# Kernel optimization log

Hardware: AMD Instinct MI355X
Metric: run time of the kernel (lower is better)

Reference implementation:

```python
import jax, jax.numpy as jnp
import numpy as np

U = 512  # units

def hard_sigmoid(x):
    # Keras hard_sigmoid: clip(0.2*x + 0.5, 0, 1)
    return jnp.clip(0.2 * x + 0.5, 0.0, 1.0)

def setup_inputs() -> dict:
    key = jax.random.key(0)
    ks = jax.random.split(key, 9)
    B, T, A, D = 64, 2048, 512, 512  # batch, annotation steps, annotation units, input dim
    s = lambda k, shape, scale: jax.random.normal(k, shape, jnp.float32) * scale
    return {
        "inputs": s(ks[0], (B, D), 1.0),
        "h": s(ks[1], (B, U), 1.0),
        "c": s(ks[2], (B, U), 1.0),
        "annotations": s(ks[3], (B, T, A), 1.0),
        "kernel": s(ks[4], (D + A, 4 * U), 0.02),
        "recurrent_kernel": s(ks[5], (U, 4 * U), 0.02),
        "bias": jnp.zeros((6 * U,), jnp.float32).at[U:2 * U].set(1.0),  # unit_forget_bias
        "kernel_u": s(ks[6], (A, U), 0.02),
        "kernel_w": s(ks[7], (U, U), 0.02),
        "kernel_v": s(ks[8], (U,), 0.02),
    }

def reference(inputs, h, c, annotations, kernel, recurrent_kernel, bias, kernel_u, kernel_w, kernel_v):
    bias_u = bias[4 * U:5 * U]
    # precomputed annotation projection (done once in build()): [B,T,U]
    uh = jnp.einsum('bta,au->btu', annotations, kernel_u) + bias_u
    # Bahdanau attention scores
    Wxstm = h @ kernel_w                                   # [B,U]
    et = jnp.einsum('btu,u->bt', jnp.tanh(uh + Wxstm[:, None, :]), kernel_v)
    at = jax.nn.softmax(et, axis=1)                        # exp/sum in source == softmax
    context = jnp.einsum('bt,bta->ba', at, annotations)    # [B,A]
    x = jnp.concatenate([inputs, context], axis=-1)        # [B, D+A]
    z = x @ kernel + h @ recurrent_kernel + bias[:4 * U]   # [B,4U]
    i = hard_sigmoid(z[:, :U])
    f = hard_sigmoid(z[:, U:2 * U])
    c_new = f * c + i * jnp.tanh(z[:, 2 * U:3 * U])
    o = hard_sigmoid(z[:, 3 * U:])
    h_new = o * jnp.tanh(c_new)
    return h_new
```

## Files before the change

### kernel.cpp

```cpp
#include <hip/hip_runtime.h>

constexpr int U = 512;
constexpr int B = 64;
constexpr int T = 2048;
constexpr int A = 512;

typedef __attribute__((ext_vector_type(8))) short short8;
typedef __attribute__((ext_vector_type(4))) float f32x4;

__device__ __forceinline__ unsigned short f32_to_bf16(float f) {
    unsigned int b = __float_as_uint(f);
    unsigned int r = (b + 0x7FFFu + ((b >> 16) & 1u)) >> 16;
    return (unsigned short)r;
}

__device__ __forceinline__ float fast_tanh(float x) {
    float e = exp2f(x * 2.885390081777927f);
    return (e - 1.0f) * __builtin_amdgcn_rcpf(e + 1.0f);
}

__device__ __forceinline__ float hard_sigmoid(float z) {
    return fminf(fmaxf(0.2f * z + 0.5f, 0.0f), 1.0f);
}

__global__ __launch_bounds__(256) void k_prep_s(const float* __restrict__ h,
                                                const float* __restrict__ kw,
                                                float* __restrict__ Sp) {
    int b = blockIdx.x >> 2;
    int kc = blockIdx.x & 3;
    int u = threadIdx.x;
    const float* hb = h + b * U + kc * 128;
    const float* kwb = kw + (size_t)kc * 128 * U;
    float a0 = 0.f, a1 = 0.f;
#pragma unroll 4
    for (int k = 0; k < 128; ++k) {
        float hv = hb[k];
        a0 += hv * kwb[(size_t)k * U + u];
        a1 += hv * kwb[(size_t)k * U + u + 256];
    }
    float* p = Sp + ((size_t)kc * 64 + b) * U;
    p[u] = a0;
    p[u + 256] = a1;
}

__global__ __launch_bounds__(256) void k_s_reduce(const float* __restrict__ Sp,
                                                  const float* __restrict__ bias,
                                                  float* __restrict__ S) {
    int gid = blockIdx.x * 256 + threadIdx.x;
    int b = gid >> 9, u = gid & 511;
    float s = bias[4 * U + u];
#pragma unroll
    for (int kc = 0; kc < 4; ++kc) s += Sp[((size_t)kc * 64 + b) * U + u];
    S[gid] = s;
}

__global__ __launch_bounds__(256) void k_prep_kut(const float* __restrict__ ku,
                                                  unsigned short* __restrict__ kut) {
    __shared__ float tile[32][33];
    int a0 = (blockIdx.x >> 4) << 5;
    int u0 = (blockIdx.x & 15) << 5;
    int c = threadIdx.x & 31, r0 = threadIdx.x >> 5;
#pragma unroll
    for (int p = 0; p < 4; ++p) {
        int r = r0 + p * 8;
        tile[r][c] = ku[(a0 + r) * U + u0 + c];
    }
    __syncthreads();
#pragma unroll
    for (int p = 0; p < 4; ++p) {
        int r = r0 + p * 8;
        kut[(u0 + r) * A + a0 + c] = f32_to_bf16(tile[c][r]);
    }
}

__global__ __launch_bounds__(256) void k_prep_wt(const float* __restrict__ kern,
                                                 const float* __restrict__ rk,
                                                 unsigned short* __restrict__ Wt) {
    __shared__ float tile[32][33];
    int k0 = blockIdx.x << 5;
    int j0 = blockIdx.y << 5;
    int c = threadIdx.x & 31, r0 = threadIdx.x >> 5;
#pragma unroll
    for (int p = 0; p < 4; ++p) {
        int r = r0 + p * 8;
        int k = k0 + r;
        float val = (k < 1024) ? kern[k * 2048 + j0 + c]
                               : rk[(k - 1024) * 2048 + j0 + c];
        tile[r][c] = val;
    }
    __syncthreads();
#pragma unroll
    for (int p = 0; p < 4; ++p) {
        int r = r0 + p * 8;
        Wt[(size_t)(j0 + r) * 1536 + k0 + c] = f32_to_bf16(tile[c][r]);
    }
}

__global__ __launch_bounds__(256, 2) void k_gemm_et(const float* __restrict__ ann,
                                                    const unsigned short* __restrict__ kut,
                                                    const float* __restrict__ S,
                                                    const float* __restrict__ v,
                                                    float* __restrict__ etp) {
    __shared__ unsigned short As[128 * 64];
    __shared__ unsigned short Bs[256 * 64];
    __shared__ float red[4][64];

    const int tid = threadIdx.x;
    const int wave = tid >> 6;
    const int lane = tid & 63;
    const int lanelo = lane & 15;
    const int quad = lane >> 4;
    const int wm = wave >> 1, wn = wave & 1;

    const int bid = blockIdx.x;
    const int nt = (bid >> 3) & 1;
    const int mt = (bid & 7) | ((bid >> 4) << 3);
    const int b = mt >> 4;
    const float* aBase = ann + (size_t)mt * 128 * A;
    const unsigned short* bBase = kut + (size_t)nt * 256 * A;

    f32x4 acc[4][8];
#pragma unroll
    for (int i = 0; i < 4; ++i)
#pragma unroll
        for (int j = 0; j < 8; ++j) acc[i][j] = {0.f, 0.f, 0.f, 0.f};

    for (int k0 = 0; k0 < A; k0 += 64) {
#pragma unroll
        for (int p = 0; p < 8; ++p) {
            int seg = p * 4 + wave;
            int flat = seg * 1024 + lane * 16;
            int row = flat >> 7;
            int sc = (flat >> 4) & 7;
            int d = sc ^ (row & 7);
            __builtin_amdgcn_global_load_lds(
                (const __attribute__((address_space(1))) void*)(bBase + (size_t)row * A + k0 + d * 8),
                (__attribute__((address_space(3))) void*)((char*)Bs + seg * 1024),
                16, 0, 0);
        }
#pragma unroll
        for (int p = 0; p < 4; ++p) {
            int flat8 = p * 256 + tid;
            int row = flat8 >> 3;
            int c8 = flat8 & 7;
            const float* src = aBase + (size_t)row * A + k0 + c8 * 8;
            f32x4 v0 = *(const f32x4*)src;
            f32x4 v1 = *(const f32x4*)(src + 4);
            short8 pk;
            pk[0] = (short)f32_to_bf16(v0.x);
            pk[1] = (short)f32_to_bf16(v0.y);
            pk[2] = (short)f32_to_bf16(v0.z);
            pk[3] = (short)f32_to_bf16(v0.w);
            pk[4] = (short)f32_to_bf16(v1.x);
            pk[5] = (short)f32_to_bf16(v1.y);
            pk[6] = (short)f32_to_bf16(v1.z);
            pk[7] = (short)f32_to_bf16(v1.w);
            *(short8*)&As[row * 64 + ((c8 ^ (row & 7)) * 8)] = pk;
        }
        __syncthreads();
#pragma unroll
        for (int s = 0; s < 2; ++s) {
            int c = s * 4 + quad;
            short8 af[4];
#pragma unroll
            for (int mi = 0; mi < 4; ++mi) {
                int row = wm * 64 + mi * 16 + lanelo;
                af[mi] = *(const short8*)&As[row * 64 + ((c ^ (row & 7)) * 8)];
            }
            short8 bfr[8];
#pragma unroll
            for (int ni = 0; ni < 8; ++ni) {
                int rowb = wn * 128 + ni * 16 + lanelo;
                bfr[ni] = *(const short8*)&Bs[rowb * 64 + ((c ^ (rowb & 7)) * 8)];
            }
#pragma unroll
            for (int mi = 0; mi < 4; ++mi)
#pragma unroll
                for (int ni = 0; ni < 8; ++ni)
                    acc[mi][ni] = __builtin_amdgcn_mfma_f32_16x16x32_bf16(
                        af[mi], bfr[ni], acc[mi][ni], 0, 0, 0);
        }
        __syncthreads();
    }

    float rows[16];
#pragma unroll
    for (int i = 0; i < 16; ++i) rows[i] = 0.f;
#pragma unroll
    for (int ni = 0; ni < 8; ++ni) {
        int n = nt * 256 + wn * 128 + ni * 16 + lanelo;
        float sv = S[b * U + n];
        float vv = v[n];
#pragma unroll
        for (int mi = 0; mi < 4; ++mi)
#pragma unroll
            for (int r = 0; r < 4; ++r)
                rows[mi * 4 + r] += fast_tanh(acc[mi][ni][r] + sv) * vv;
    }
#pragma unroll
    for (int i = 0; i < 16; ++i) {
        rows[i] += __shfl_xor(rows[i], 1);
        rows[i] += __shfl_xor(rows[i], 2);
        rows[i] += __shfl_xor(rows[i], 4);
        rows[i] += __shfl_xor(rows[i], 8);
    }
    if (lanelo == 0) {
#pragma unroll
        for (int mi = 0; mi < 4; ++mi)
#pragma unroll
            for (int r = 0; r < 4; ++r)
                red[wave][mi * 16 + quad * 4 + r] = rows[mi * 4 + r];
    }
    __syncthreads();
    if (tid < 128) {
        int wmv = tid >> 6, ml = tid & 63;
        float sum = red[wmv * 2][ml] + red[wmv * 2 + 1][ml];
        etp[(size_t)nt * (1024 * 128) + (size_t)mt * 128 + tid] = sum;
    }
}

__global__ __launch_bounds__(256) void k_softmax(const float* __restrict__ etp,
                                                 float* __restrict__ at) {
    __shared__ float sred[256];
    int b = blockIdx.x;
    const float* e = etp + b * T;
    float vals[8];
    float mx = -1e30f;
#pragma unroll
    for (int i = 0; i < 8; ++i) {
        int t = threadIdx.x + i * 256;
        float x = e[t] + e[131072 + t];
        vals[i] = x;
        mx = fmaxf(mx, x);
    }
    sred[threadIdx.x] = mx;
    __syncthreads();
    for (int s = 128; s > 0; s >>= 1) {
        if (threadIdx.x < s) sred[threadIdx.x] = fmaxf(sred[threadIdx.x], sred[threadIdx.x + s]);
        __syncthreads();
    }
    mx = sred[0];
    __syncthreads();
    float sum = 0.f;
#pragma unroll
    for (int i = 0; i < 8; ++i) {
        float x = exp2f((vals[i] - mx) * 1.4426950408889634f);
        vals[i] = x;
        sum += x;
    }
    sred[threadIdx.x] = sum;
    __syncthreads();
    for (int s = 128; s > 0; s >>= 1) {
        if (threadIdx.x < s) sred[threadIdx.x] += sred[threadIdx.x + s];
        __syncthreads();
    }
    float inv = 1.0f / sred[0];
#pragma unroll
    for (int i = 0; i < 8; ++i) at[b * T + threadIdx.x + i * 256] = vals[i] * inv;
}

__global__ __launch_bounds__(256) void k_ctx_part(const float* __restrict__ at,
                                                  const float* __restrict__ ann,
                                                  float* __restrict__ part) {
    __shared__ float buf[2][512];
    int b = blockIdx.x >> 3;
    int tc = blockIdx.x & 7;
    int half = threadIdx.x >> 7;
    int a4 = (threadIdx.x & 127) << 2;
    const float* annb = ann + ((size_t)b * T + tc * 256) * A;
    const float* atb = at + b * T + tc * 256;
    f32x4 acc = {0.f, 0.f, 0.f, 0.f};
    for (int t = half; t < 256; t += 2) {
        float w = atb[t];
        f32x4 rv = *(const f32x4*)(annb + (size_t)t * A + a4);
        acc.x += w * rv.x;
        acc.y += w * rv.y;
        acc.z += w * rv.z;
        acc.w += w * rv.w;
    }
    *(f32x4*)&buf[half][a4] = acc;
    __syncthreads();
    int a2 = threadIdx.x << 1;
    float s0 = buf[0][a2] + buf[1][a2];
    float s1 = buf[0][a2 + 1] + buf[1][a2 + 1];
    float* p = part + ((size_t)b * 8 + tc) * A;
    p[a2] = s0;
    p[a2 + 1] = s1;
}

__global__ __launch_bounds__(256) void k_ctx_reduce(const float* __restrict__ part,
                                                    float* __restrict__ ctx) {
    int b = blockIdx.x;
    for (int a = threadIdx.x; a < A; a += 256) {
        float s = 0.f;
#pragma unroll
        for (int c = 0; c < 8; ++c) s += part[((size_t)b * 8 + c) * A + a];
        ctx[b * A + a] = s;
    }
}

__global__ __launch_bounds__(256) void k_prep_xb(const float* __restrict__ inputs,
                                                 const float* __restrict__ ctx,
                                                 const float* __restrict__ h,
                                                 unsigned short* __restrict__ xb) {
    int b = blockIdx.y;
    int k = blockIdx.x * 256 + threadIdx.x;
    float val;
    if (k < 512) val = inputs[b * 512 + k];
    else if (k < 1024) val = ctx[b * 512 + (k - 512)];
    else val = h[b * 512 + (k - 1024)];
    xb[b * 1536 + k] = f32_to_bf16(val);
}

__global__ __launch_bounds__(256) void k_zgemm(const unsigned short* __restrict__ xb,
                                               const unsigned short* __restrict__ Wt,
                                               float* __restrict__ zpart) {
    const int kc = blockIdx.x & 7;
    const int nt = blockIdx.x >> 3;
    const int wave = threadIdx.x >> 6;
    const int lane = threadIdx.x & 63;
    const int lanelo = lane & 15;
    const int quad = lane >> 4;

    const int n = nt * 64 + wave * 16 + lanelo;
    const unsigned short* bp = Wt + (size_t)n * 1536 + kc * 192 + quad * 8;
    const unsigned short* ap = xb + (size_t)lanelo * 1536 + kc * 192 + quad * 8;

    f32x4 acc[4];
#pragma unroll
    for (int i = 0; i < 4; ++i) acc[i] = {0.f, 0.f, 0.f, 0.f};

#pragma unroll
    for (int ks = 0; ks < 6; ++ks) {
        short8 bfrag = *(const short8*)(bp + ks * 32);
#pragma unroll
        for (int mi = 0; mi < 4; ++mi) {
            short8 afrag = *(const short8*)(ap + (size_t)mi * 16 * 1536 + ks * 32);
            acc[mi] = __builtin_amdgcn_mfma_f32_16x16x32_bf16(afrag, bfrag, acc[mi], 0, 0, 0);
        }
    }

    float* p = zpart + (size_t)kc * 64 * 2048;
#pragma unroll
    for (int mi = 0; mi < 4; ++mi)
#pragma unroll
        for (int r = 0; r < 4; ++r) {
            int m = mi * 16 + quad * 4 + r;
            p[(size_t)m * 2048 + n] = acc[mi][r];
        }
}

__global__ __launch_bounds__(256) void k_gates(const float* __restrict__ zpart,
                                               const float* __restrict__ bias,
                                               const float* __restrict__ c,
                                               float* __restrict__ hnew) {
    int gid = blockIdx.x * 256 + threadIdx.x;
    int b = gid >> 9;
    int u = gid & 511;
    float z[4];
#pragma unroll
    for (int g = 0; g < 4; ++g) {
        int j = (g << 9) + u;
        float s = bias[j];
#pragma unroll
        for (int kc = 0; kc < 8; ++kc)
            s += zpart[((size_t)kc * 64 + b) * 2048 + j];
        z[g] = s;
    }
    float ig = hard_sigmoid(z[0]);
    float fg = hard_sigmoid(z[1]);
    float cn = fg * c[b * 512 + u] + ig * fast_tanh(z[2]);
    float og = hard_sigmoid(z[3]);
    hnew[b * 512 + u] = og * fast_tanh(cn);
}

extern "C" void kernel_launch(void* const* d_in, const int* in_sizes, int n_in,
                              void* d_out, int out_size, void* d_ws, size_t ws_size,
                              hipStream_t stream) {
    const float* inputs = (const float*)d_in[0];
    const float* h      = (const float*)d_in[1];
    const float* c      = (const float*)d_in[2];
    const float* ann    = (const float*)d_in[3];
    const float* kern   = (const float*)d_in[4];
    const float* rk     = (const float*)d_in[5];
    const float* bias   = (const float*)d_in[6];
    const float* ku     = (const float*)d_in[7];
    const float* kw     = (const float*)d_in[8];
    const float* kv     = (const float*)d_in[9];

    char* ws = (char*)d_ws;
    float*          S     = (float*)(ws + 0);
    unsigned short* kut   = (unsigned short*)(ws + 131072);
    float*          etp   = (float*)(ws + 655360);
    float*          at    = (float*)(ws + 1703936);
    float*          part  = (float*)(ws + 2228224);
    float*          Sp    = (float*)(ws + 2228224);
    float*          ctx   = (float*)(ws + 3276800);
    unsigned short* xb    = (unsigned short*)(ws + 3407872);
    unsigned short* Wt    = (unsigned short*)(ws + 3604480);
    float*          zpart = (float*)(ws + 9895936);
    float*          hnew  = (float*)d_out;

    k_prep_wt<<<dim3(48, 64), 256, 0, stream>>>(kern, rk, Wt);
    k_prep_kut<<<256, 256, 0, stream>>>(ku, kut);
    k_prep_s<<<256, 256, 0, stream>>>(h, kw, Sp);
    k_s_reduce<<<128, 256, 0, stream>>>(Sp, bias, S);
    k_gemm_et<<<2048, 256, 0, stream>>>(ann, kut, S, kv, etp);
    k_softmax<<<64, 256, 0, stream>>>(etp, at);
    k_ctx_part<<<64 * 8, 256, 0, stream>>>(at, ann, part);
    k_ctx_reduce<<<64, 256, 0, stream>>>(part, ctx);
    k_prep_xb<<<dim3(6, 64), 256, 0, stream>>>(inputs, ctx, h, xb);
    k_zgemm<<<256, 256, 0, stream>>>(xb, Wt, zpart);
    k_gates<<<128, 256, 0, stream>>>(zpart, bias, c, hnew);
}
```

Baseline: 516.7 us.

## Retile attention-score GEMM to full-N 64-row tiles with register prefetch

The et GEMM now gives each block 64 annotation rows against all 512 units instead of 128 rows against half the units. Each annotation row is therefore read and converted to bf16 only once, and the two-way partial score sum is gone, so softmax reads a single et buffer. The next k-slice of annotations is also prefetched into registers so the global load overlaps the MFMA loop. The cost is that the full kernel_u tile (64 KB of LDS) is now reloaded per block, and more LDS per block may reduce occupancy.

```diff
diff --git a/kernel.cpp b/kernel.cpp
--- a/kernel.cpp
+++ b/kernel.cpp
@@ -100,9 +100,9 @@
                                                     const unsigned short* __restrict__ kut,
                                                     const float* __restrict__ S,
                                                     const float* __restrict__ v,
-                                                    float* __restrict__ etp) {
-    __shared__ unsigned short As[128 * 64];
-    __shared__ unsigned short Bs[256 * 64];
+                                                    float* __restrict__ et) {
+    __shared__ unsigned short As[64 * 64];
+    __shared__ unsigned short Bs[512 * 64];
     __shared__ float red[4][64];
 
     const int tid = threadIdx.x;
@@ -110,14 +110,12 @@
     const int lane = tid & 63;
     const int lanelo = lane & 15;
     const int quad = lane >> 4;
-    const int wm = wave >> 1, wn = wave & 1;
-
-    const int bid = blockIdx.x;
-    const int nt = (bid >> 3) & 1;
-    const int mt = (bid & 7) | ((bid >> 4) << 3);
-    const int b = mt >> 4;
-    const float* aBase = ann + (size_t)mt * 128 * A;
-    const unsigned short* bBase = kut + (size_t)nt * 256 * A;
+    const int wn = wave;
+
+    const int mt = blockIdx.x;
+    const int b = mt >> 5;
+    const int t0 = (mt & 31) << 6;
+    const float* aBase = ann + (size_t)mt * 64 * A;
 
     f32x4 acc[4][8];
 #pragma unroll
@@ -125,27 +123,34 @@
 #pragma unroll
         for (int j = 0; j < 8; ++j) acc[i][j] = {0.f, 0.f, 0.f, 0.f};
 
+    f32x4 pv[4];
+    const int rowA = tid >> 3;
+    const int c8A = tid & 7;
+
+#pragma unroll
+    for (int q = 0; q < 2; ++q) {
+        const float* src = aBase + (size_t)(q * 32 + rowA) * A + 0 + c8A * 8;
+        pv[q * 2] = *(const f32x4*)src;
+        pv[q * 2 + 1] = *(const f32x4*)(src + 4);
+    }
+
     for (int k0 = 0; k0 < A; k0 += 64) {
 #pragma unroll
-        for (int p = 0; p < 8; ++p) {
+        for (int p = 0; p < 16; ++p) {
             int seg = p * 4 + wave;
             int flat = seg * 1024 + lane * 16;
             int row = flat >> 7;
             int sc = (flat >> 4) & 7;
             int d = sc ^ (row & 7);
             __builtin_amdgcn_global_load_lds(
-                (const __attribute__((address_space(1))) void*)(bBase + (size_t)row * A + k0 + d * 8),
+                (const __attribute__((address_space(1))) void*)(kut + (size_t)row * A + k0 + d * 8),
                 (__attribute__((address_space(3))) void*)((char*)Bs + seg * 1024),
                 16, 0, 0);
         }
 #pragma unroll
-        for (int p = 0; p < 4; ++p) {
-            int flat8 = p * 256 + tid;
-            int row = flat8 >> 3;
-            int c8 = flat8 & 7;
-            const float* src = aBase + (size_t)row * A + k0 + c8 * 8;
-            f32x4 v0 = *(const f32x4*)src;
-            f32x4 v1 = *(const f32x4*)(src + 4);
+        for (int q = 0; q < 2; ++q) {
+            int row = q * 32 + rowA;
+            f32x4 v0 = pv[q * 2], v1 = pv[q * 2 + 1];
             short8 pk;
             pk[0] = (short)f32_to_bf16(v0.x);
             pk[1] = (short)f32_to_bf16(v0.y);
@@ -155,16 +160,24 @@
             pk[5] = (short)f32_to_bf16(v1.y);
             pk[6] = (short)f32_to_bf16(v1.z);
             pk[7] = (short)f32_to_bf16(v1.w);
-            *(short8*)&As[row * 64 + ((c8 ^ (row & 7)) * 8)] = pk;
+            *(short8*)&As[row * 64 + ((c8A ^ (row & 7)) * 8)] = pk;
         }
         __syncthreads();
+        if (k0 + 64 < A) {
+#pragma unroll
+            for (int q = 0; q < 2; ++q) {
+                const float* src = aBase + (size_t)(q * 32 + rowA) * A + (k0 + 64) + c8A * 8;
+                pv[q * 2] = *(const f32x4*)src;
+                pv[q * 2 + 1] = *(const f32x4*)(src + 4);
+            }
+        }
 #pragma unroll
         for (int s = 0; s < 2; ++s) {
             int c = s * 4 + quad;
             short8 af[4];
 #pragma unroll
             for (int mi = 0; mi < 4; ++mi) {
-                int row = wm * 64 + mi * 16 + lanelo;
+                int row = mi * 16 + lanelo;
                 af[mi] = *(const short8*)&As[row * 64 + ((c ^ (row & 7)) * 8)];
             }
             short8 bfr[8];
@@ -188,9 +201,9 @@
     for (int i = 0; i < 16; ++i) rows[i] = 0.f;
 #pragma unroll
     for (int ni = 0; ni < 8; ++ni) {
-        int n = nt * 256 + wn * 128 + ni * 16 + lanelo;
-        float sv = S[b * U + n];
-        float vv = v[n];
+        int u = wn * 128 + ni * 16 + lanelo;
+        float sv = S[b * U + u];
+        float vv = v[u];
 #pragma unroll
         for (int mi = 0; mi < 4; ++mi)
 #pragma unroll
@@ -212,24 +225,23 @@
                 red[wave][mi * 16 + quad * 4 + r] = rows[mi * 4 + r];
     }
     __syncthreads();
-    if (tid < 128) {
-        int wmv = tid >> 6, ml = tid & 63;
-        float sum = red[wmv * 2][ml] + red[wmv * 2 + 1][ml];
-        etp[(size_t)nt * (1024 * 128) + (size_t)mt * 128 + tid] = sum;
-    }
-}
-
-__global__ __launch_bounds__(256) void k_softmax(const float* __restrict__ etp,
+    if (tid < 64) {
+        float sum = red[0][tid] + red[1][tid] + red[2][tid] + red[3][tid];
+        et[b * T + t0 + tid] = sum;
+    }
+}
+
+__global__ __launch_bounds__(256) void k_softmax(const float* __restrict__ et,
                                                  float* __restrict__ at) {
     __shared__ float sred[256];
     int b = blockIdx.x;
-    const float* e = etp + b * T;
+    const float* e = et + b * T;
     float vals[8];
     float mx = -1e30f;
 #pragma unroll
     for (int i = 0; i < 8; ++i) {
         int t = threadIdx.x + i * 256;
-        float x = e[t] + e[131072 + t];
+        float x = e[t];
         vals[i] = x;
         mx = fmaxf(mx, x);
     }
@@ -391,7 +403,7 @@
     char* ws = (char*)d_ws;
     float*          S     = (float*)(ws + 0);
     unsigned short* kut   = (unsigned short*)(ws + 131072);
-    float*          etp   = (float*)(ws + 655360);
+    float*          et    = (float*)(ws + 655360);
     float*          at    = (float*)(ws + 1703936);
     float*          part  = (float*)(ws + 2228224);
     float*          Sp    = (float*)(ws + 2228224);
@@ -405,8 +417,8 @@
     k_prep_kut<<<256, 256, 0, stream>>>(ku, kut);
     k_prep_s<<<256, 256, 0, stream>>>(h, kw, Sp);
     k_s_reduce<<<128, 256, 0, stream>>>(Sp, bias, S);
-    k_gemm_et<<<2048, 256, 0, stream>>>(ann, kut, S, kv, etp);
-    k_softmax<<<64, 256, 0, stream>>>(etp, at);
+    k_gemm_et<<<2048, 256, 0, stream>>>(ann, kut, S, kv, et);
+    k_softmax<<<64, 256, 0, stream>>>(et, at);
     k_ctx_part<<<64 * 8, 256, 0, stream>>>(at, ann, part);
     k_ctx_reduce<<<64, 256, 0, stream>>>(part, ctx);
     k_prep_xb<<<dim3(6, 64), 256, 0, stream>>>(inputs, ctx, h, xb);
```

After: 515.6 us. No clear change (-0.2%).
